# Optimization experiments

Hardware: AMD Instinct MI355X
Metric: run time of the kernel (lower is better)

Reference implementation:

```python
import jax, jax.numpy as jnp
import numpy as np

N_NODES = 100000
N_EDGES = 3200000
IN_DIM, HID, OUT_DIM = 128, 64, 32
N_LAYERS = 3


def setup_inputs() -> dict:
    key = jax.random.key(0)
    ks = jax.random.split(key, 10)
    x = jax.random.normal(ks[0], (N_NODES, IN_DIM), dtype=jnp.float32)
    edge_index = jax.random.randint(ks[1], (2, N_EDGES), 0, N_NODES, dtype=jnp.int64)
    edge_weight = jax.random.uniform(ks[2], (N_EDGES,), dtype=jnp.float32)
    s_in = 1.0 / np.sqrt(IN_DIM)
    s_h = 1.0 / np.sqrt(HID)
    W_in = jax.random.uniform(ks[3], (IN_DIM, HID), jnp.float32, -s_in, s_in)
    b_in = jax.random.uniform(ks[4], (HID,), jnp.float32, -s_in, s_in)
    W_g = jax.random.uniform(ks[5], (N_LAYERS, HID, HID), jnp.float32, -s_h, s_h)
    b_g = jax.random.uniform(ks[6], (N_LAYERS, HID), jnp.float32, -s_h, s_h)
    W_out = jax.random.uniform(ks[7], (HID, OUT_DIM), jnp.float32, -s_h, s_h)
    b_out = jax.random.uniform(ks[8], (OUT_DIM,), jnp.float32, -s_h, s_h)
    return {"x": x, "edge_index": edge_index, "edge_weight": edge_weight,
            "W_in": W_in, "b_in": b_in, "W_g": W_g, "b_g": b_g,
            "W_out": W_out, "b_out": b_out}


def reference(x, edge_index, edge_weight, W_in, b_in, W_g, b_g, W_out, b_out):
    # input projection: [N, IN_DIM] -> [N, HID]
    h = x @ W_in + b_in
    src = edge_index[0]
    dst = edge_index[1]
    num_nodes = h.shape[0]
    for l in range(N_LAYERS):
        # per-edge message: gather source features, scale by edge weight
        msg = h[src] * edge_weight[:, None]          # [E, HID]
        agg = jax.ops.segment_sum(msg, dst, num_segments=num_nodes)  # [N, HID]
        h = jax.nn.relu((h + agg) @ W_g[l] + b_g[l])
    return h @ W_out + b_out
```

## Files before the change

kernel.cpp:

```cpp
#include <hip/hip_runtime.h>
#include <hip/hip_bf16.h>
#include <hip/hip_fp16.h>

#define N_NODES 100000
#define IN_DIM 128
#define HID 64
#define OUT_DIM 32
#define BUCK 128
#define NB 782
#define CAP 5120
#define AST 68
#define CHUNK 8192

typedef float floatx2 __attribute__((ext_vector_type(2)));

__device__ __forceinline__ unsigned int pack4_fp8(float f0, float f1, float f2, float f3) {
    int u = __builtin_amdgcn_cvt_pk_fp8_f32(f0, f1, 0, false);
    u     = __builtin_amdgcn_cvt_pk_fp8_f32(f2, f3, u, true);
    return (unsigned int)u;
}

__global__ __launch_bounds__(512) void k_part(const int* __restrict__ src,
                                              const int* __restrict__ dst,
                                              const float* __restrict__ ew,
                                              int* __restrict__ bcur,
                                              unsigned int* __restrict__ ed, int E) {
    __shared__ int cnt[NB];
    __shared__ int lscan[NB];
    __shared__ int base[NB];
    __shared__ unsigned int stage[CHUNK];
    const int tid = threadIdx.x;
    const int lo = blockIdx.x * CHUNK;
    const int hi = min(E, lo + CHUNK);

    for (int i = tid; i < NB; i += 512) cnt[i] = 0;
    __syncthreads();
    for (int e = lo + tid; e < hi; e += 512)
        atomicAdd(&cnt[dst[e] >> 7], 1);
    __syncthreads();
    {
        const int i0 = tid, i1 = tid + 512;
        if (i0 < NB) lscan[i0] = cnt[i0];
        if (i1 < NB) lscan[i1] = cnt[i1];
        __syncthreads();
        for (int d = 1; d < 1024; d <<= 1) {
            int v0 = 0, v1 = 0;
            if (i0 >= d && i0 < NB) v0 = lscan[i0 - d];
            if (i1 >= d && i1 < NB) v1 = lscan[i1 - d];
            __syncthreads();
            if (i0 < NB) lscan[i0] += v0;
            if (i1 < NB) lscan[i1] += v1;
            __syncthreads();
        }
    }
    for (int i = tid; i < NB; i += 512) {
        int c = cnt[i];
        lscan[i] -= c;
        base[i] = c ? atomicAdd(&bcur[i], c) : 0;
        cnt[i] = 0;
    }
    __syncthreads();
    for (int e = lo + tid; e < hi; e += 512) {
        int d  = dst[e];
        int bk = d >> 7;
        unsigned int q = (unsigned int)(ew[e] * 256.0f);
        if (q > 255u) q = 255u;
        int r = atomicAdd(&cnt[bk], 1);
        stage[lscan[bk] + r] = (unsigned int)src[e]
                               | ((unsigned int)(d & 127) << 17) | (q << 24);
    }
    __syncthreads();
    for (int b = tid; b < NB; b += 512) {
        int c = cnt[b];
        if (!c) continue;
        int room = CAP - base[b];
        int m = c < room ? c : (room > 0 ? room : 0);
        const unsigned int* s = &stage[lscan[b]];
        unsigned int* g = ed + (size_t)b * CAP + base[b];
        for (int i = 0; i < m; ++i) g[i] = s[i];
    }
}

__global__ __launch_bounds__(512) void k_sort(const unsigned int* __restrict__ ed,
                                              unsigned int* __restrict__ ed2,
                                              const int* __restrict__ bcur,
                                              int* __restrict__ off,
                                              int* __restrict__ endo) {
    __shared__ int cnt[BUCK];
    __shared__ int inc[BUCK];
    __shared__ int cur[BUCK];
    const int tid = threadIdx.x;
    const int bkt = blockIdx.x;
    const int b0 = bkt * CAP;
    const int b1 = b0 + min(bcur[bkt], CAP);

    if (tid < BUCK) cnt[tid] = 0;
    __syncthreads();
    for (int i = b0 + tid; i < b1; i += 512)
        atomicAdd(&cnt[(ed[i] >> 17) & 127], 1);
    __syncthreads();
    if (tid < BUCK) inc[tid] = cnt[tid];
    __syncthreads();
    for (int d = 1; d < BUCK; d <<= 1) {
        int v = 0;
        if (tid < BUCK && tid >= d) v = inc[tid - d];
        __syncthreads();
        if (tid < BUCK) inc[tid] += v;
        __syncthreads();
    }
    if (tid < BUCK) {
        int ex = inc[tid] - cnt[tid];
        cur[tid] = ex;
        int n = bkt * BUCK + tid;
        if (n < N_NODES) {
            off[n]  = b0 + ex;
            endo[n] = b0 + ex + cnt[tid];
        }
    }
    __syncthreads();
    for (int i = b0 + tid; i < b1; i += 512) {
        unsigned int e = ed[i];
        int dl = (e >> 17) & 127;
        int p = atomicAdd(&cur[dl], 1);
        ed2[b0 + p] = e;
    }
}

__global__ __launch_bounds__(256) void k_proj0(const float* __restrict__ x,
                                               const float* __restrict__ W_in,
                                               const float* __restrict__ b_in,
                                               const float* __restrict__ Wg0,
                                               unsigned int* __restrict__ g0) {
    __shared__ float xt[64][AST];
    const int tid = threadIdx.x;
    const int n0 = blockIdx.x * 64;
    const int nq = tid >> 4, jq = tid & 15;
    const int nb = nq * 4, jb = jq * 4;
    const float4 bj = *(const float4*)(b_in + jb);
    float acc[4][4];
#pragma unroll
    for (int ni = 0; ni < 4; ++ni) {
        acc[ni][0] = bj.x; acc[ni][1] = bj.y; acc[ni][2] = bj.z; acc[ni][3] = bj.w;
    }

    for (int half = 0; half < 2; ++half) {
        __syncthreads();
        for (int i = tid; i < 64 * 16; i += 256) {
            int r = i >> 4;
            int c4 = (i & 15) * 4;
            float4 v = make_float4(0.f, 0.f, 0.f, 0.f);
            int n = n0 + r;
            if (n < N_NODES) v = *(const float4*)(x + (size_t)n * IN_DIM + half * 64 + c4);
            xt[c4 + 0][r] = v.x;
            xt[c4 + 1][r] = v.y;
            xt[c4 + 2][r] = v.z;
            xt[c4 + 3][r] = v.w;
        }
        __syncthreads();
#pragma unroll 4
        for (int k = 0; k < 64; ++k) {
            const float4 a = *(const float4*)&xt[k][nb];
            const float4 w = *(const float4*)&W_in[(half * 64 + k) * HID + jb];
            acc[0][0] = fmaf(a.x, w.x, acc[0][0]); acc[0][1] = fmaf(a.x, w.y, acc[0][1]);
            acc[0][2] = fmaf(a.x, w.z, acc[0][2]); acc[0][3] = fmaf(a.x, w.w, acc[0][3]);
            acc[1][0] = fmaf(a.y, w.x, acc[1][0]); acc[1][1] = fmaf(a.y, w.y, acc[1][1]);
            acc[1][2] = fmaf(a.y, w.z, acc[1][2]); acc[1][3] = fmaf(a.y, w.w, acc[1][3]);
            acc[2][0] = fmaf(a.z, w.x, acc[2][0]); acc[2][1] = fmaf(a.z, w.y, acc[2][1]);
            acc[2][2] = fmaf(a.z, w.z, acc[2][2]); acc[2][3] = fmaf(a.z, w.w, acc[2][3]);
            acc[3][0] = fmaf(a.w, w.x, acc[3][0]); acc[3][1] = fmaf(a.w, w.y, acc[3][1]);
            acc[3][2] = fmaf(a.w, w.z, acc[3][2]); acc[3][3] = fmaf(a.w, w.w, acc[3][3]);
        }
    }
    __syncthreads();
#pragma unroll
    for (int ni = 0; ni < 4; ++ni) {
        const bool valid = (n0 + nb + ni) < N_NODES;
#pragma unroll
        for (int f = 0; f < 4; ++f)
            xt[jb + f][nb + ni] = valid ? acc[ni][f] : 0.0f;
    }
    __syncthreads();
    float c2[4][4];
#pragma unroll
    for (int ni = 0; ni < 4; ++ni)
        c2[ni][0] = c2[ni][1] = c2[ni][2] = c2[ni][3] = 0.0f;
#pragma unroll 4
    for (int k = 0; k < HID; ++k) {
        const float4 a = *(const float4*)&xt[k][nb];
        const float4 w = *(const float4*)&Wg0[k * HID + jb];
        c2[0][0] = fmaf(a.x, w.x, c2[0][0]); c2[0][1] = fmaf(a.x, w.y, c2[0][1]);
        c2[0][2] = fmaf(a.x, w.z, c2[0][2]); c2[0][3] = fmaf(a.x, w.w, c2[0][3]);
        c2[1][0] = fmaf(a.y, w.x, c2[1][0]); c2[1][1] = fmaf(a.y, w.y, c2[1][1]);
        c2[1][2] = fmaf(a.y, w.z, c2[1][2]); c2[1][3] = fmaf(a.y, w.w, c2[1][3]);
        c2[2][0] = fmaf(a.z, w.x, c2[2][0]); c2[2][1] = fmaf(a.z, w.y, c2[2][1]);
        c2[2][2] = fmaf(a.z, w.z, c2[2][2]); c2[2][3] = fmaf(a.z, w.w, c2[2][3]);
        c2[3][0] = fmaf(a.w, w.x, c2[3][0]); c2[3][1] = fmaf(a.w, w.y, c2[3][1]);
        c2[3][2] = fmaf(a.w, w.z, c2[3][2]); c2[3][3] = fmaf(a.w, w.w, c2[3][3]);
    }
#pragma unroll
    for (int ni = 0; ni < 4; ++ni) {
        int n = n0 + nb + ni;
        if (n < N_NODES)
            g0[(size_t)n * 16 + jq] = pack4_fp8(c2[ni][0], c2[ni][1],
                                                c2[ni][2], c2[ni][3]);
    }
}

#define ROW(p)  (gp[((size_t)((p) & 0x1FFFFu)) * 8])
#define WT(p)   (((float)((p) >> 24) + 0.5f) * 0.00390625f)
#define ACC(p, v) do { const float w_ = WT(p); const floatx2 w2 = {w_, w_};     \
        A01 += w2 * __builtin_amdgcn_cvt_pk_f32_fp8((v).x, false);              \
        A23 += w2 * __builtin_amdgcn_cvt_pk_f32_fp8((v).x, true);               \
        A45 += w2 * __builtin_amdgcn_cvt_pk_f32_fp8((v).y, false);              \
        A67 += w2 * __builtin_amdgcn_cvt_pk_f32_fp8((v).y, true); } while (0)

#define AGG_GATHER_BODY                                                        \
    floatx2 A01 = {0.f, 0.f}, A23 = {0.f, 0.f},                                \
            A45 = {0.f, 0.f}, A67 = {0.f, 0.f};                                \
    if (valid) {                                                               \
        uint2 sv = gp[(size_t)n * 8];                                          \
        A01 = __builtin_amdgcn_cvt_pk_f32_fp8(sv.x, false);                    \
        A23 = __builtin_amdgcn_cvt_pk_f32_fp8(sv.x, true);                     \
        A45 = __builtin_amdgcn_cvt_pk_f32_fp8(sv.y, false);                    \
        A67 = __builtin_amdgcn_cvt_pk_f32_fp8(sv.y, true);                     \
        int i = off[n];                                                        \
        const int i1 = endo[n];                                                \
        if (i + 4 <= i1) {                                                     \
            unsigned int p0 = ed2[i], p1 = ed2[i+1], p2 = ed2[i+2], p3 = ed2[i+3]; \
            uint2 v0 = ROW(p0), v1 = ROW(p1), v2 = ROW(p2), v3 = ROW(p3);      \
            i += 4;                                                            \
            for (; i + 4 <= i1; i += 4) {                                      \
                unsigned int q0 = ed2[i], q1 = ed2[i+1], q2 = ed2[i+2], q3 = ed2[i+3]; \
                uint2 w0 = ROW(q0), w1 = ROW(q1), w2 = ROW(q2), w3 = ROW(q3);  \
                ACC(p0, v0); ACC(p1, v1); ACC(p2, v2); ACC(p3, v3);            \
                p0 = q0; p1 = q1; p2 = q2; p3 = q3;                            \
                v0 = w0; v1 = w1; v2 = w2; v3 = w3;                            \
            }                                                                  \
            ACC(p0, v0); ACC(p1, v1); ACC(p2, v2); ACC(p3, v3);                \
        }                                                                      \
        for (; i < i1; ++i) { unsigned int p = ed2[i]; uint2 v = ROW(p); ACC(p, v); } \
    }                                                                          \
    const float a0 = A01.x, a1 = A01.y, a2 = A23.x, a3 = A23.y,                \
                a4 = A45.x, a5 = A45.y, a6 = A67.x, a7 = A67.y;

__global__ __launch_bounds__(512) void k_agg_mid(
        const unsigned int* __restrict__ g_in,
        unsigned int* __restrict__ g_out,
        const unsigned int* __restrict__ ed2,
        const int* __restrict__ off, const int* __restrict__ endo,
        const float* __restrict__ bg, const float* __restrict__ Wnext) {
    __shared__ float sHT[HID][AST];
    __shared__ float sW[HID * HID];
    const int tid = threadIdx.x;
    const int grp = tid >> 3, l8 = tid & 7;
    const int n = blockIdx.x * 64 + grp;
    const bool valid = (n < N_NODES);
    const uint2* gp = (const uint2*)g_in + l8;

    for (int i = tid; i < HID * HID; i += 512) sW[i] = Wnext[i];

    AGG_GATHER_BODY

    const float4 bA = *(const float4*)(bg + l8 * 8);
    const float4 bB = *(const float4*)(bg + l8 * 8 + 4);
    const int f0 = l8 * 8;
    sHT[f0 + 0][grp] = valid ? fmaxf(a0 + bA.x, 0.f) : 0.f;
    sHT[f0 + 1][grp] = valid ? fmaxf(a1 + bA.y, 0.f) : 0.f;
    sHT[f0 + 2][grp] = valid ? fmaxf(a2 + bA.z, 0.f) : 0.f;
    sHT[f0 + 3][grp] = valid ? fmaxf(a3 + bA.w, 0.f) : 0.f;
    sHT[f0 + 4][grp] = valid ? fmaxf(a4 + bB.x, 0.f) : 0.f;
    sHT[f0 + 5][grp] = valid ? fmaxf(a5 + bB.y, 0.f) : 0.f;
    sHT[f0 + 6][grp] = valid ? fmaxf(a6 + bB.z, 0.f) : 0.f;
    sHT[f0 + 7][grp] = valid ? fmaxf(a7 + bB.w, 0.f) : 0.f;
    __syncthreads();

    const int npr = tid >> 4;
    const int jq  = tid & 15;
    const int jb  = jq * 4;
    float c0[4] = {0.f, 0.f, 0.f, 0.f};
    float c1[4] = {0.f, 0.f, 0.f, 0.f};
#pragma unroll 4
    for (int k = 0; k < HID; ++k) {
        const float2 a = *(const float2*)&sHT[k][npr * 2];
        const float4 w = *(const float4*)&sW[k * HID + jb];
        c0[0] = fmaf(a.x, w.x, c0[0]); c0[1] = fmaf(a.x, w.y, c0[1]);
        c0[2] = fmaf(a.x, w.z, c0[2]); c0[3] = fmaf(a.x, w.w, c0[3]);
        c1[0] = fmaf(a.y, w.x, c1[0]); c1[1] = fmaf(a.y, w.y, c1[1]);
        c1[2] = fmaf(a.y, w.z, c1[2]); c1[3] = fmaf(a.y, w.w, c1[3]);
    }
    const int nbase = blockIdx.x * 64 + npr * 2;
    if (nbase < N_NODES)
        g_out[(size_t)nbase * 16 + jq] = pack4_fp8(c0[0], c0[1], c0[2], c0[3]);
    if (nbase + 1 < N_NODES)
        g_out[(size_t)(nbase + 1) * 16 + jq] = pack4_fp8(c1[0], c1[1], c1[2], c1[3]);
}

__global__ __launch_bounds__(512) void k_agg_out(
        const unsigned int* __restrict__ g_in,
        float* __restrict__ out,
        const unsigned int* __restrict__ ed2,
        const int* __restrict__ off, const int* __restrict__ endo,
        const float* __restrict__ bg, const float* __restrict__ W_out,
        const float* __restrict__ b_out) {
    __shared__ float sHT[HID][AST];
    __shared__ float sW[HID * OUT_DIM];
    const int tid = threadIdx.x;
    const int grp = tid >> 3, l8 = tid & 7;
    const int n = blockIdx.x * 64 + grp;
    const bool valid = (n < N_NODES);
    const uint2* gp = (const uint2*)g_in + l8;

    for (int i = tid; i < HID * OUT_DIM; i += 512) sW[i] = W_out[i];

    AGG_GATHER_BODY

    const float4 bA = *(const float4*)(bg + l8 * 8);
    const float4 bB = *(const float4*)(bg + l8 * 8 + 4);
    const int f0 = l8 * 8;
    sHT[f0 + 0][grp] = valid ? fmaxf(a0 + bA.x, 0.f) : 0.f;
    sHT[f0 + 1][grp] = valid ? fmaxf(a1 + bA.y, 0.f) : 0.f;
    sHT[f0 + 2][grp] = valid ? fmaxf(a2 + bA.z, 0.f) : 0.f;
    sHT[f0 + 3][grp] = valid ? fmaxf(a3 + bA.w, 0.f) : 0.f;
    sHT[f0 + 4][grp] = valid ? fmaxf(a4 + bB.x, 0.f) : 0.f;
    sHT[f0 + 5][grp] = valid ? fmaxf(a5 + bB.y, 0.f) : 0.f;
    sHT[f0 + 6][grp] = valid ? fmaxf(a6 + bB.z, 0.f) : 0.f;
    sHT[f0 + 7][grp] = valid ? fmaxf(a7 + bB.w, 0.f) : 0.f;
    __syncthreads();

    const int node = tid >> 3;
    const int jb   = (tid & 7) * 4;
    const float4 bo = *(const float4*)(b_out + jb);
    float c4[4] = {bo.x, bo.y, bo.z, bo.w};
#pragma unroll 4
    for (int k = 0; k < HID; ++k) {
        const float a = sHT[k][node];
        const float4 w = *(const float4*)&sW[k * OUT_DIM + jb];
        c4[0] = fmaf(a, w.x, c4[0]); c4[1] = fmaf(a, w.y, c4[1]);
        c4[2] = fmaf(a, w.z, c4[2]); c4[3] = fmaf(a, w.w, c4[3]);
    }
    const int n2 = blockIdx.x * 64 + node;
    if (n2 < N_NODES)
        *(float4*)(out + (size_t)n2 * OUT_DIM + jb) =
            make_float4(c4[0], c4[1], c4[2], c4[3]);
}

#undef ROW
#undef WT
#undef ACC
#undef AGG_GATHER_BODY

extern "C" void kernel_launch(void* const* d_in, const int* in_sizes, int n_in,
                              void* d_out, int out_size, void* d_ws, size_t ws_size,
                              hipStream_t stream) {
    const float* x     = (const float*)d_in[0];
    const int*   ei    = (const int*)d_in[1];
    const float* ew    = (const float*)d_in[2];
    const float* W_in  = (const float*)d_in[3];
    const float* b_in  = (const float*)d_in[4];
    const float* W_g   = (const float*)d_in[5];
    const float* b_g   = (const float*)d_in[6];
    const float* W_out = (const float*)d_in[7];
    const float* b_out = (const float*)d_in[8];
    float* out = (float*)d_out;

    const int E = in_sizes[2];
    const int* src = ei;
    const int* dst = ei + E;

    char* ws = (char*)d_ws;
    unsigned int* ed  = (unsigned int*)ws;
    unsigned int* ed2 = ed + (size_t)NB * CAP;
    unsigned int* gA  = ed2 + (size_t)NB * CAP;
    unsigned int* gB  = gA + (size_t)N_NODES * 16;
    int* misc = (int*)(gB + (size_t)N_NODES * 16);
    int* off  = misc;
    int* endo = misc + 100032;
    int* bcur = misc + 200064;

    const int nparts = (E + CHUNK - 1) / CHUNK;

    hipMemsetAsync(bcur, 0, NB * sizeof(int), stream);
    k_part<<<nparts, 512, 0, stream>>>(src, dst, ew, bcur, ed, E);
    k_sort<<<NB, 512, 0, stream>>>(ed, ed2, bcur, off, endo);

    k_proj0<<<(N_NODES + 63) / 64, 256, 0, stream>>>(x, W_in, b_in, W_g, gA);

    k_agg_mid<<<(N_NODES + 63) / 64, 512, 0, stream>>>(
        gA, gB, ed2, off, endo, b_g + 0 * HID, W_g + 1 * HID * HID);
    k_agg_mid<<<(N_NODES + 63) / 64, 512, 0, stream>>>(
        gB, gA, ed2, off, endo, b_g + 1 * HID, W_g + 2 * HID * HID);
    k_agg_out<<<(N_NODES + 63) / 64, 512, 0, stream>>>(
        gA, out, ed2, off, endo, b_g + 2 * HID, W_out, b_out);
}
```

Measured before the change: 378.6 us.

## Fold W_in into first layer weights and run projection on bf16 MFMA

A tiny new kernel precomputes W_in·Wg0 (and b_in·Wg0) as a bf16 transposed matrix, so the node projection becomes a single 128→64 matmul instead of two chained FP32 GEMMs. k_proj0 now converts x rows to bf16 and uses 16x16x32 bf16 MFMA instructions, staging results through shared memory before packing to fp8. The combined weights live in the edge-partition workspace, so projection is moved before partitioning. This cuts FP32 FMA work and shared-memory transposes at the cost of bf16 rounding of x and the weights and one extra small launch.

Result: faster. 348.7 us (-7.9%).

```diff
diff --git a/kernel.cpp b/kernel.cpp
--- a/kernel.cpp
+++ b/kernel.cpp
@@ -13,11 +13,18 @@
 #define CHUNK 8192
 
 typedef float floatx2 __attribute__((ext_vector_type(2)));
+typedef short bf16x8 __attribute__((ext_vector_type(8)));
+typedef float f32x4 __attribute__((ext_vector_type(4)));
 
 __device__ __forceinline__ unsigned int pack4_fp8(float f0, float f1, float f2, float f3) {
     int u = __builtin_amdgcn_cvt_pk_fp8_f32(f0, f1, 0, false);
     u     = __builtin_amdgcn_cvt_pk_fp8_f32(f2, f3, u, true);
     return (unsigned int)u;
+}
+
+__device__ __forceinline__ unsigned short f2bf(float f) {
+    unsigned int u = __float_as_uint(f);
+    return (unsigned short)((u + 0x7FFFu + ((u >> 16) & 1u)) >> 16);
 }
 
 __global__ __launch_bounds__(512) void k_part(const int* __restrict__ src,
@@ -126,83 +133,109 @@
     }
 }
 
+__global__ __launch_bounds__(256) void k_wc(const float* __restrict__ W_in,
+                                            const float* __restrict__ b_in,
+                                            const float* __restrict__ Wg0,
+                                            unsigned short* __restrict__ wct,
+                                            float* __restrict__ bc) {
+    __shared__ float sWg[HID * HID];
+    __shared__ float sWi[16 * HID];
+    const int tid = threadIdx.x;
+    const int k0 = blockIdx.x * 16;
+    for (int i = tid; i < HID * HID; i += 256) sWg[i] = Wg0[i];
+    for (int i = tid; i < 16 * HID; i += 256) sWi[i] = W_in[k0 * HID + i];
+    __syncthreads();
+    const int kr = tid >> 4;
+    const int jb = (tid & 15) * 4;
+    float c0 = 0.f, c1 = 0.f, c2 = 0.f, c3 = 0.f;
+#pragma unroll 4
+    for (int m = 0; m < HID; ++m) {
+        const float a = sWi[kr * HID + m];
+        const float4 wv = *(const float4*)&sWg[m * HID + jb];
+        c0 = fmaf(a, wv.x, c0); c1 = fmaf(a, wv.y, c1);
+        c2 = fmaf(a, wv.z, c2); c3 = fmaf(a, wv.w, c3);
+    }
+    const int k = k0 + kr;
+    wct[(size_t)(jb + 0) * IN_DIM + k] = f2bf(c0);
+    wct[(size_t)(jb + 1) * IN_DIM + k] = f2bf(c1);
+    wct[(size_t)(jb + 2) * IN_DIM + k] = f2bf(c2);
+    wct[(size_t)(jb + 3) * IN_DIM + k] = f2bf(c3);
+    if (blockIdx.x == 0 && tid < HID) {
+        float s = 0.f;
+        for (int m = 0; m < HID; ++m) s = fmaf(b_in[m], sWg[m * HID + tid], s);
+        bc[tid] = s;
+    }
+}
+
 __global__ __launch_bounds__(256) void k_proj0(const float* __restrict__ x,
-                                               const float* __restrict__ W_in,
-                                               const float* __restrict__ b_in,
-                                               const float* __restrict__ Wg0,
+                                               const unsigned short* __restrict__ wct,
+                                               const float* __restrict__ bc,
                                                unsigned int* __restrict__ g0) {
-    __shared__ float xt[64][AST];
-    const int tid = threadIdx.x;
-    const int n0 = blockIdx.x * 64;
-    const int nq = tid >> 4, jq = tid & 15;
-    const int nb = nq * 4, jb = jq * 4;
-    const float4 bj = *(const float4*)(b_in + jb);
-    float acc[4][4];
-#pragma unroll
-    for (int ni = 0; ni < 4; ++ni) {
-        acc[ni][0] = bj.x; acc[ni][1] = bj.y; acc[ni][2] = bj.z; acc[ni][3] = bj.w;
-    }
-
-    for (int half = 0; half < 2; ++half) {
-        __syncthreads();
-        for (int i = tid; i < 64 * 16; i += 256) {
-            int r = i >> 4;
-            int c4 = (i & 15) * 4;
-            float4 v = make_float4(0.f, 0.f, 0.f, 0.f);
-            int n = n0 + r;
-            if (n < N_NODES) v = *(const float4*)(x + (size_t)n * IN_DIM + half * 64 + c4);
-            xt[c4 + 0][r] = v.x;
-            xt[c4 + 1][r] = v.y;
-            xt[c4 + 2][r] = v.z;
-            xt[c4 + 3][r] = v.w;
+    __shared__ float sH[4][32][76];
+    const int tid = threadIdx.x;
+    const int w = tid >> 6, lane = tid & 63;
+    const int lr = lane & 15, lg = lane >> 4;
+    const int nb0 = blockIdx.x * 128 + w * 32;
+
+    bf16x8 B[4][4];
+#pragma unroll
+    for (int j = 0; j < 4; ++j)
+#pragma unroll
+        for (int c = 0; c < 4; ++c)
+            B[j][c] = *(const bf16x8*)(wct + (16 * j + lr) * IN_DIM + 32 * c + 8 * lg);
+
+    f32x4 acc[2][4];
+#pragma unroll
+    for (int mt = 0; mt < 2; ++mt)
+#pragma unroll
+        for (int j = 0; j < 4; ++j)
+            acc[mt][j] = (f32x4){0.f, 0.f, 0.f, 0.f};
+
+#pragma unroll
+    for (int mt = 0; mt < 2; ++mt) {
+        int n = nb0 + mt * 16 + lr;
+        if (n >= N_NODES) n = N_NODES - 1;
+        const float* xr = x + (size_t)n * IN_DIM + 8 * lg;
+        bf16x8 A[4];
+#pragma unroll
+        for (int c = 0; c < 4; ++c) {
+            const float4 lo = *(const float4*)(xr + 32 * c);
+            const float4 hi = *(const float4*)(xr + 32 * c + 4);
+            bf16x8 a;
+            a[0] = (short)f2bf(lo.x); a[1] = (short)f2bf(lo.y);
+            a[2] = (short)f2bf(lo.z); a[3] = (short)f2bf(lo.w);
+            a[4] = (short)f2bf(hi.x); a[5] = (short)f2bf(hi.y);
+            a[6] = (short)f2bf(hi.z); a[7] = (short)f2bf(hi.w);
+            A[c] = a;
         }
-        __syncthreads();
-#pragma unroll 4
-        for (int k = 0; k < 64; ++k) {
-            const float4 a = *(const float4*)&xt[k][nb];
-            const float4 w = *(const float4*)&W_in[(half * 64 + k) * HID + jb];
-            acc[0][0] = fmaf(a.x, w.x, acc[0][0]); acc[0][1] = fmaf(a.x, w.y, acc[0][1]);
-            acc[0][2] = fmaf(a.x, w.z, acc[0][2]); acc[0][3] = fmaf(a.x, w.w, acc[0][3]);
-            acc[1][0] = fmaf(a.y, w.x, acc[1][0]); acc[1][1] = fmaf(a.y, w.y, acc[1][1]);
-            acc[1][2] = fmaf(a.y, w.z, acc[1][2]); acc[1][3] = fmaf(a.y, w.w, acc[1][3]);
-            acc[2][0] = fmaf(a.z, w.x, acc[2][0]); acc[2][1] = fmaf(a.z, w.y, acc[2][1]);
-            acc[2][2] = fmaf(a.z, w.z, acc[2][2]); acc[2][3] = fmaf(a.z, w.w, acc[2][3]);
-            acc[3][0] = fmaf(a.w, w.x, acc[3][0]); acc[3][1] = fmaf(a.w, w.y, acc[3][1]);
-            acc[3][2] = fmaf(a.w, w.z, acc[3][2]); acc[3][3] = fmaf(a.w, w.w, acc[3][3]);
+#pragma unroll
+        for (int j = 0; j < 4; ++j)
+#pragma unroll
+            for (int c = 0; c < 4; ++c)
+                acc[mt][j] = __builtin_amdgcn_mfma_f32_16x16x32_bf16(
+                    A[c], B[j][c], acc[mt][j], 0, 0, 0);
+    }
+
+#pragma unroll
+    for (int j = 0; j < 4; ++j) {
+        const float bj = bc[16 * j + lr];
+#pragma unroll
+        for (int mt = 0; mt < 2; ++mt)
+#pragma unroll
+            for (int r = 0; r < 4; ++r)
+                sH[w][mt * 16 + 4 * lg + r][16 * j + lr] = acc[mt][j][r] + bj;
+    }
+    __syncthreads();
+
+#pragma unroll
+    for (int i = 0; i < 8; ++i) {
+        const int idx = lane + 64 * i;
+        const int nl = idx >> 4, jq = idx & 15;
+        const int n = nb0 + nl;
+        if (n < N_NODES) {
+            const float4 v = *(const float4*)&sH[w][nl][jq * 4];
+            g0[(size_t)n * 16 + jq] = pack4_fp8(v.x, v.y, v.z, v.w);
         }
-    }
-    __syncthreads();
-#pragma unroll
-    for (int ni = 0; ni < 4; ++ni) {
-        const bool valid = (n0 + nb + ni) < N_NODES;
-#pragma unroll
-        for (int f = 0; f < 4; ++f)
-            xt[jb + f][nb + ni] = valid ? acc[ni][f] : 0.0f;
-    }
-    __syncthreads();
-    float c2[4][4];
-#pragma unroll
-    for (int ni = 0; ni < 4; ++ni)
-        c2[ni][0] = c2[ni][1] = c2[ni][2] = c2[ni][3] = 0.0f;
-#pragma unroll 4
-    for (int k = 0; k < HID; ++k) {
-        const float4 a = *(const float4*)&xt[k][nb];
-        const float4 w = *(const float4*)&Wg0[k * HID + jb];
-        c2[0][0] = fmaf(a.x, w.x, c2[0][0]); c2[0][1] = fmaf(a.x, w.y, c2[0][1]);
-        c2[0][2] = fmaf(a.x, w.z, c2[0][2]); c2[0][3] = fmaf(a.x, w.w, c2[0][3]);
-        c2[1][0] = fmaf(a.y, w.x, c2[1][0]); c2[1][1] = fmaf(a.y, w.y, c2[1][1]);
-        c2[1][2] = fmaf(a.y, w.z, c2[1][2]); c2[1][3] = fmaf(a.y, w.w, c2[1][3]);
-        c2[2][0] = fmaf(a.z, w.x, c2[2][0]); c2[2][1] = fmaf(a.z, w.y, c2[2][1]);
-        c2[2][2] = fmaf(a.z, w.z, c2[2][2]); c2[2][3] = fmaf(a.z, w.w, c2[2][3]);
-        c2[3][0] = fmaf(a.w, w.x, c2[3][0]); c2[3][1] = fmaf(a.w, w.y, c2[3][1]);
-        c2[3][2] = fmaf(a.w, w.z, c2[3][2]); c2[3][3] = fmaf(a.w, w.w, c2[3][3]);
-    }
-#pragma unroll
-    for (int ni = 0; ni < 4; ++ni) {
-        int n = n0 + nb + ni;
-        if (n < N_NODES)
-            g0[(size_t)n * 16 + jq] = pack4_fp8(c2[ni][0], c2[ni][1],
-                                                c2[ni][2], c2[ni][3]);
     }
 }
 
@@ -379,11 +412,15 @@
 
     const int nparts = (E + CHUNK - 1) / CHUNK;
 
+    unsigned short* wct = (unsigned short*)ed;
+    float* bcv = (float*)(ed + 4096);
+
+    k_wc<<<8, 256, 0, stream>>>(W_in, b_in, W_g, wct, bcv);
+    k_proj0<<<(N_NODES + 127) / 128, 256, 0, stream>>>(x, wct, bcv, gA);
+
     hipMemsetAsync(bcur, 0, NB * sizeof(int), stream);
     k_part<<<nparts, 512, 0, stream>>>(src, dst, ew, bcur, ed, E);
     k_sort<<<NB, 512, 0, stream>>>(ed, ed2, bcur, off, endo);
-
-    k_proj0<<<(N_NODES + 63) / 64, 256, 0, stream>>>(x, W_in, b_in, W_g, gA);
 
     k_agg_mid<<<(N_NODES + 63) / 64, 512, 0, stream>>>(
         gA, gB, ed2, off, endo, b_g + 0 * HID, W_g + 1 * HID * HID);
```
